# Performance work log

Measured on AMD Instinct MI355X. Metric: run time of the kernel, lower is better.

The kernel has to match this reference:

```python
import jax, jax.numpy as jnp
import numpy as np

NEG_INF = -1e9
LRELU_SLOPE = 0.2

B, C, FIN, FOUT = 8, 2048, 128, 64


def setup_inputs() -> dict:
    key = jax.random.key(0)
    k1, k2, k3, k4 = jax.random.split(key, 4)
    H = jax.random.normal(k1, (B, C, FIN), dtype=jnp.float32)
    A = jax.random.randint(k2, (B, C, C), 0, 2, dtype=jnp.int32)
    W = jax.random.normal(k3, (FIN, FOUT), dtype=jnp.float32)
    a = jax.random.normal(k4, (2 * FOUT,), dtype=jnp.float32)
    return {"H": H, "A": A, "W": W, "a": a}


def reference(H, A, W, a):
    # Wh: [B, C, F]
    Wh = jnp.einsum("bcf,fo->bco", H, W)
    F = Wh.shape[-1]
    a1, a2 = a[:F], a[F:]
    # e_ij = a . concat(Wh_i, Wh_j) = (Wh_i . a1) + (Wh_j . a2)
    # -> never materialize the (B,C,C,2F) concat tensor; same math.
    s1 = jnp.einsum("bcf,f->bc", Wh, a1)  # [B, C] contribution of node i
    s2 = jnp.einsum("bcf,f->bc", Wh, a2)  # [B, C] contribution of node j
    e = jax.nn.leaky_relu(s1[:, :, None] + s2[:, None, :], LRELU_SLOPE)  # [B,C,C]
    mask = (A > 0) | jnp.eye(A.shape[-1], dtype=bool)[None]
    e = jnp.where(mask, e, NEG_INF)
    alpha = jax.nn.softmax(e, axis=-1)
    # dropout omitted (eval mode) for a deterministic correctness baseline
    out = jax.nn.relu(jnp.einsum("bij,bjf->bif", alpha, Wh))
    return out
```

## Files before the change

kernel.cpp:

```cpp
#include <hip/hip_runtime.h>

#define NB 8
#define NC 2048
#define KIN 128
#define NF 64

#define WTSTRIDE 136
#define RSTRIDE 68
#define MOFF 60.0f
#define LOG2E 1.44269504088896340736f

typedef float floatx4_t __attribute__((ext_vector_type(4)));
typedef __bf16 bf16x8_t __attribute__((ext_vector_type(8)));
typedef unsigned short ushort8_t __attribute__((ext_vector_type(8)));

static __device__ __forceinline__ unsigned short f2bf(float f) {
  union { float f; unsigned int u; } v; v.f = f;
  unsigned int u = v.u;
  u += 0x7FFFu + ((u >> 16) & 1u);
  return (unsigned short)(u >> 16);
}

static __device__ __forceinline__ float lrelu(float x) {
  return fmaxf(x, 0.2f * x);
}

__global__ __launch_bounds__(256, 4) void k1_prep(
    const float* __restrict__ H, const float* __restrict__ W,
    const float* __restrict__ avec,
    float* __restrict__ s1g, float* __restrict__ s2g,
    unsigned short* __restrict__ WhT)
{
  __shared__ unsigned short WTsh[NF * WTSTRIDE];
  __shared__ float w1sh[KIN];
  __shared__ float w2sh[KIN];

  const int t = threadIdx.x;
  const int b = blockIdx.x >> 7;
  const int c0 = (blockIdx.x & 127) * 16;

  for (int i = t; i < KIN * NF; i += 256) {
    int k = i >> 6, f = i & 63;
    WTsh[f * WTSTRIDE + k] = f2bf(W[i]);
  }
  if (t < KIN) {
    float acc1 = 0.f, acc2 = 0.f;
    const float* wr = W + t * NF;
#pragma unroll
    for (int f = 0; f < NF; ++f) {
      float wv = wr[f];
      acc1 += wv * avec[f];
      acc2 += wv * avec[NF + f];
    }
    w1sh[t] = acc1;
    w2sh[t] = acc2;
  }
  __syncthreads();

  {
    const int r = t >> 4;
    const int x = t & 15;
    const float* hp = H + (size_t)(b * NC + c0 + r) * KIN + x * 8;
    float4 h0 = *(const float4*)(hp);
    float4 h1 = *(const float4*)(hp + 4);
    float4 u10 = *(const float4*)(w1sh + x * 8);
    float4 u11 = *(const float4*)(w1sh + x * 8 + 4);
    float4 u20 = *(const float4*)(w2sh + x * 8);
    float4 u21 = *(const float4*)(w2sh + x * 8 + 4);
    float p1 = h0.x * u10.x + h0.y * u10.y + h0.z * u10.z + h0.w * u10.w
             + h1.x * u11.x + h1.y * u11.y + h1.z * u11.z + h1.w * u11.w;
    float p2 = h0.x * u20.x + h0.y * u20.y + h0.z * u20.z + h0.w * u20.w
             + h1.x * u21.x + h1.y * u21.y + h1.z * u21.z + h1.w * u21.w;
#pragma unroll
    for (int off = 1; off < 16; off <<= 1) {
      p1 += __shfl_xor(p1, off);
      p2 += __shfl_xor(p2, off);
    }
    if (x == 0) {
      s1g[b * NC + c0 + r] = p1;
      s2g[b * NC + c0 + r] = p2;
    }
  }

  const int wave = t >> 6;
  const int lane = t & 63;
  const int m = lane & 15;
  const int q = lane >> 4;
  floatx4_t acc = (floatx4_t){0.f, 0.f, 0.f, 0.f};

  const float* hb = H + (size_t)(b * NC + c0 + m) * KIN;
#pragma unroll
  for (int kt = 0; kt < 4; ++kt) {
    const int kbase = kt * 32 + q * 8;
    float4 h0 = *(const float4*)(hb + kbase);
    float4 h1 = *(const float4*)(hb + kbase + 4);
    ushort8_t bu;
    bu[0] = f2bf(h0.x); bu[1] = f2bf(h0.y); bu[2] = f2bf(h0.z); bu[3] = f2bf(h0.w);
    bu[4] = f2bf(h1.x); bu[5] = f2bf(h1.y); bu[6] = f2bf(h1.z); bu[7] = f2bf(h1.w);
    bf16x8_t bf = __builtin_bit_cast(bf16x8_t, bu);
    ushort8_t au = *(const ushort8_t*)(WTsh + (wave * 16 + m) * WTSTRIDE + kbase);
    bf16x8_t af = __builtin_bit_cast(bf16x8_t, au);
    acc = __builtin_amdgcn_mfma_f32_16x16x32_bf16(af, bf, acc, 0, 0, 0);
  }
#pragma unroll
  for (int i2 = 0; i2 < 4; ++i2) {
    const int f = wave * 16 + q * 4 + i2;
    WhT[(size_t)(b * NF + f) * NC + c0 + m] = f2bf(acc[i2]);
  }
}

__global__ __launch_bounds__(256, 4) void k2_attn(
    const int* __restrict__ A, const float* __restrict__ s1g,
    const float* __restrict__ s2g, const unsigned short* __restrict__ WhT,
    float* __restrict__ out)
{
  __shared__ float s2_sh[NC];
  __shared__ float s1_sh[16];
  __shared__ float wmax_sh[4];
  __shared__ float red_sh[4 * 16 * RSTRIDE];
  __shared__ float lsum_sh[4 * 16];

  const int t = threadIdx.x;
  const int b = blockIdx.x >> 7;
  const int i0 = (blockIdx.x & 127) * 16;
  const int wave = t >> 6;
  const int lane = t & 63;

  float lmax;
  {
    const float* sp = s2g + b * NC;
    float4 v0 = *(const float4*)(sp + t * 4);
    float4 v1 = *(const float4*)(sp + 1024 + t * 4);
    *(float4*)(s2_sh + t * 4) = v0;
    *(float4*)(s2_sh + 1024 + t * 4) = v1;
    lmax = fmaxf(fmaxf(fmaxf(v0.x, v0.y), fmaxf(v0.z, v0.w)),
                 fmaxf(fmaxf(v1.x, v1.y), fmaxf(v1.z, v1.w)));
#pragma unroll
    for (int off = 1; off < 64; off <<= 1)
      lmax = fmaxf(lmax, __shfl_xor(lmax, off));
    if (lane == 0) wmax_sh[wave] = lmax;
  }
  if (t < 16) s1_sh[t] = s1g[b * NC + i0 + t];
  __syncthreads();

  const float s2max =
      fmaxf(fmaxf(wmax_sh[0], wmax_sh[1]), fmaxf(wmax_sh[2], wmax_sh[3]));

  const int m = lane & 15;
  const int q = lane >> 4;
  const int gi = i0 + m;
  const float s1m = s1_sh[m];
  const float mmL = (lrelu(s1m + s2max) - MOFF) * LOG2E;
  const int* Ap = A + ((size_t)b * NC + gi) * NC;
  const unsigned short* whb = WhT + (size_t)b * NF * NC;

  ushort8_t ou;
  {
    const unsigned short ov = (m == 0) ? (unsigned short)0x3F80 : (unsigned short)0;
#pragma unroll
    for (int idx = 0; idx < 8; ++idx) ou[idx] = ov;
  }
  const bf16x8_t onesf = __builtin_bit_cast(bf16x8_t, ou);

  floatx4_t acc[4], accl;
#pragma unroll
  for (int nt = 0; nt < 4; ++nt) acc[nt] = (floatx4_t){0.f, 0.f, 0.f, 0.f};
  accl = (floatx4_t){0.f, 0.f, 0.f, 0.f};

  const int ktBeg = wave * 16;
  int4 abuf[2][2];
  {
    const int* ap0 = Ap + ktBeg * 32 + q * 8;
    abuf[0][0] = *(const int4*)ap0;
    abuf[0][1] = *(const int4*)(ap0 + 4);
    const int* ap1 = ap0 + 32;
    abuf[1][0] = *(const int4*)ap1;
    abuf[1][1] = *(const int4*)(ap1 + 4);
  }

#pragma unroll 2
  for (int kk = 0; kk < 16; ++kk) {
    const int kt = ktBeg + kk;
    const int jq = kt * 32 + q * 8;
    const int cur = kk & 1;
    const int4 a0 = abuf[cur][0];
    const int4 a1 = abuf[cur][1];
    if (kk + 2 < 16) {
      const int* ap = Ap + (kt + 2) * 32 + q * 8;
      abuf[cur][0] = *(const int4*)ap;
      abuf[cur][1] = *(const int4*)(ap + 4);
    }
    ushort8_t whc[4];
#pragma unroll
    for (int nt = 0; nt < 4; ++nt)
      whc[nt] = *(const ushort8_t*)(whb + (size_t)(nt * 16 + m) * NC + jq);

    float4 s0 = *(const float4*)(s2_sh + jq);
    float4 s1v = *(const float4*)(s2_sh + jq + 4);
    const float sv[8] = {s0.x, s0.y, s0.z, s0.w, s1v.x, s1v.y, s1v.z, s1v.w};
    const int av[8] = {a0.x, a0.y, a0.z, a0.w, a1.x, a1.y, a1.z, a1.w};
    const int d = gi - jq;
    unsigned int pu[8];
#pragma unroll
    for (int idx = 0; idx < 8; ++idx) {
      float x = s1m + sv[idx];
      float p = __builtin_amdgcn_exp2f(fmaf(lrelu(x), LOG2E, -mmL));
      bool keep = (av[idx] > 0) || (d == idx);
      p = keep ? p : 0.0f;
      pu[idx] = __builtin_bit_cast(unsigned int, p);
    }
    uint4 pk;
    pk.x = __builtin_amdgcn_perm(pu[1], pu[0], 0x07060302u);
    pk.y = __builtin_amdgcn_perm(pu[3], pu[2], 0x07060302u);
    pk.z = __builtin_amdgcn_perm(pu[5], pu[4], 0x07060302u);
    pk.w = __builtin_amdgcn_perm(pu[7], pu[6], 0x07060302u);
    const bf16x8_t af = __builtin_bit_cast(bf16x8_t, pk);
#pragma unroll
    for (int nt = 0; nt < 4; ++nt) {
      bf16x8_t bf = __builtin_bit_cast(bf16x8_t, whc[nt]);
      acc[nt] = __builtin_amdgcn_mfma_f32_16x16x32_bf16(af, bf, acc[nt], 0, 0, 0);
    }
    accl = __builtin_amdgcn_mfma_f32_16x16x32_bf16(af, onesf, accl, 0, 0, 0);
  }

#pragma unroll
  for (int nt = 0; nt < 4; ++nt) {
#pragma unroll
    for (int i2 = 0; i2 < 4; ++i2) {
      red_sh[wave * (16 * RSTRIDE) + (q * 4 + i2) * RSTRIDE + nt * 16 + m] =
          acc[nt][i2];
    }
  }
  if (m == 0) {
#pragma unroll
    for (int i2 = 0; i2 < 4; ++i2)
      lsum_sh[wave * 16 + q * 4 + i2] = accl[i2];
  }
  __syncthreads();

  {
    const int row = t >> 4;
    const int f0 = (t & 15) * 4;
    float4 v = {0.f, 0.f, 0.f, 0.f};
    float ls = 0.f;
#pragma unroll
    for (int w = 0; w < 4; ++w) {
      const float* rp = red_sh + w * (16 * RSTRIDE) + row * RSTRIDE + f0;
      float4 vv = *(const float4*)rp;
      v.x += vv.x; v.y += vv.y; v.z += vv.z; v.w += vv.w;
      ls += lsum_sh[w * 16 + row];
    }
    const float inv = 1.0f / ls;
    float4 o;
    o.x = fmaxf(v.x * inv, 0.f);
    o.y = fmaxf(v.y * inv, 0.f);
    o.z = fmaxf(v.z * inv, 0.f);
    o.w = fmaxf(v.w * inv, 0.f);
    *(float4*)(out + (size_t)(b * NC + i0 + row) * NF + f0) = o;
  }
}

extern "C" void kernel_launch(void* const* d_in, const int* in_sizes, int n_in,
                              void* d_out, int out_size, void* d_ws, size_t ws_size,
                              hipStream_t stream) {
  const float* H = (const float*)d_in[0];
  const int* A = (const int*)d_in[1];
  const float* W = (const float*)d_in[2];
  const float* avec = (const float*)d_in[3];
  float* out = (float*)d_out;

  char* ws = (char*)d_ws;
  unsigned short* WhT = (unsigned short*)ws;
  float* s1 = (float*)(ws + (size_t)NB * NF * NC * 2);
  float* s2 = s1 + NB * NC;

  k1_prep<<<dim3(NB * (NC / 16)), dim3(256), 0, stream>>>(H, W, avec, s1, s2, WhT);
  k2_attn<<<dim3(NB * (NC / 16)), dim3(256), 0, stream>>>(A, s1, s2, WhT, out);
}
```

Before: 232.2 us.

## Stage adjacency mask as packed bits in shared memory before attention loop

Each block now reads its 16 rows of the int32 adjacency matrix up front with coalesced full-row loads. It packs each row into a byte bitmask (diagonal included) in shared memory, and the main MFMA loop reads one mask byte per lane instead of two int4 global loads. This replaces scattered 32-byte-per-lane A loads interleaved with compute by a contiguous prologue, and drops the register double-buffering of A. The risk is that the A traffic is no longer overlapped with the exp/MFMA work, so the prologue latency becomes exposed. It also adds about 4 KB of LDS per block, which could lower occupancy.

Result: slower. 239.7 us (+3.2%).

```diff
diff --git a/kernel.cpp b/kernel.cpp
--- a/kernel.cpp
+++ b/kernel.cpp
@@ -7,6 +7,7 @@
 
 #define WTSTRIDE 136
 #define RSTRIDE 68
+#define MROW 264
 #define MOFF 60.0f
 #define LOG2E 1.44269504088896340736f
 
@@ -115,6 +116,7 @@
     float* __restrict__ out)
 {
   __shared__ float s2_sh[NC];
+  __shared__ unsigned char mask_sh[16 * MROW];
   __shared__ float s1_sh[16];
   __shared__ float wmax_sh[4];
   __shared__ float red_sh[4 * 16 * RSTRIDE];
@@ -141,6 +143,33 @@
     if (lane == 0) wmax_sh[wave] = lmax;
   }
   if (t < 16) s1_sh[t] = s1g[b * NC + i0 + t];
+
+#pragma unroll 2
+  for (int rr = 0; rr < 4; ++rr) {
+    const int row = wave * 4 + rr;
+    const int gRow = i0 + row;
+    const int* arow = A + ((size_t)b * NC + gRow) * NC;
+#pragma unroll
+    for (int span = 0; span < 4; ++span) {
+      const int cbase = span * 512 + lane * 8;
+      int4 a0 = *(const int4*)(arow + cbase);
+      int4 a1 = *(const int4*)(arow + cbase + 4);
+      unsigned int byte = 0;
+      byte |= (a0.x > 0 || cbase + 0 == gRow) ? 1u : 0u;
+      byte |= (a0.y > 0 || cbase + 1 == gRow) ? 2u : 0u;
+      byte |= (a0.z > 0 || cbase + 2 == gRow) ? 4u : 0u;
+      byte |= (a0.w > 0 || cbase + 3 == gRow) ? 8u : 0u;
+      byte |= (a1.x > 0 || cbase + 4 == gRow) ? 16u : 0u;
+      byte |= (a1.y > 0 || cbase + 5 == gRow) ? 32u : 0u;
+      byte |= (a1.z > 0 || cbase + 6 == gRow) ? 64u : 0u;
+      byte |= (a1.w > 0 || cbase + 7 == gRow) ? 128u : 0u;
+      unsigned int v = byte;
+      v |= ((unsigned int)__shfl_xor((int)v, 1)) << 8;
+      v |= ((unsigned int)__shfl_xor((int)v, 2)) << 16;
+      if ((lane & 3) == 0)
+        *(unsigned int*)(mask_sh + row * MROW + span * 64 + lane) = v;
+    }
+  }
   __syncthreads();
 
   const float s2max =
@@ -148,10 +177,8 @@
 
   const int m = lane & 15;
   const int q = lane >> 4;
-  const int gi = i0 + m;
   const float s1m = s1_sh[m];
   const float mmL = (lrelu(s1m + s2max) - MOFF) * LOG2E;
-  const int* Ap = A + ((size_t)b * NC + gi) * NC;
   const unsigned short* whb = WhT + (size_t)b * NF * NC;
 
   ushort8_t ou;
@@ -168,28 +195,10 @@
   accl = (floatx4_t){0.f, 0.f, 0.f, 0.f};
 
   const int ktBeg = wave * 16;
-  int4 abuf[2][2];
-  {
-    const int* ap0 = Ap + ktBeg * 32 + q * 8;
-    abuf[0][0] = *(const int4*)ap0;
-    abuf[0][1] = *(const int4*)(ap0 + 4);
-    const int* ap1 = ap0 + 32;
-    abuf[1][0] = *(const int4*)ap1;
-    abuf[1][1] = *(const int4*)(ap1 + 4);
-  }
-
-#pragma unroll 2
   for (int kk = 0; kk < 16; ++kk) {
     const int kt = ktBeg + kk;
     const int jq = kt * 32 + q * 8;
-    const int cur = kk & 1;
-    const int4 a0 = abuf[cur][0];
-    const int4 a1 = abuf[cur][1];
-    if (kk + 2 < 16) {
-      const int* ap = Ap + (kt + 2) * 32 + q * 8;
-      abuf[cur][0] = *(const int4*)ap;
-      abuf[cur][1] = *(const int4*)(ap + 4);
-    }
+    const unsigned int mb = mask_sh[m * MROW + kt * 4 + q];
     ushort8_t whc[4];
 #pragma unroll
     for (int nt = 0; nt < 4; ++nt)
@@ -198,22 +207,19 @@
     float4 s0 = *(const float4*)(s2_sh + jq);
     float4 s1v = *(const float4*)(s2_sh + jq + 4);
     const float sv[8] = {s0.x, s0.y, s0.z, s0.w, s1v.x, s1v.y, s1v.z, s1v.w};
-    const int av[8] = {a0.x, a0.y, a0.z, a0.w, a1.x, a1.y, a1.z, a1.w};
-    const int d = gi - jq;
-    unsigned int pu[8];
-#pragma unroll
-    for (int idx = 0; idx < 8; ++idx) {
-      float x = s1m + sv[idx];
-      float p = __builtin_amdgcn_exp2f(fmaf(lrelu(x), LOG2E, -mmL));
-      bool keep = (av[idx] > 0) || (d == idx);
-      p = keep ? p : 0.0f;
-      pu[idx] = __builtin_bit_cast(unsigned int, p);
-    }
     uint4 pk;
-    pk.x = __builtin_amdgcn_perm(pu[1], pu[0], 0x07060302u);
-    pk.y = __builtin_amdgcn_perm(pu[3], pu[2], 0x07060302u);
-    pk.z = __builtin_amdgcn_perm(pu[5], pu[4], 0x07060302u);
-    pk.w = __builtin_amdgcn_perm(pu[7], pu[6], 0x07060302u);
+#pragma unroll
+    for (int pair = 0; pair < 4; ++pair) {
+      float p0 = __builtin_amdgcn_exp2f(
+          fmaf(lrelu(s1m + sv[2 * pair]), LOG2E, -mmL));
+      float p1 = __builtin_amdgcn_exp2f(
+          fmaf(lrelu(s1m + sv[2 * pair + 1]), LOG2E, -mmL));
+      p0 = (mb & (1u << (2 * pair))) ? p0 : 0.0f;
+      p1 = (mb & (2u << (2 * pair))) ? p1 : 0.0f;
+      pk[pair] = __builtin_amdgcn_perm(__builtin_bit_cast(unsigned int, p1),
+                                       __builtin_bit_cast(unsigned int, p0),
+                                       0x07060302u);
+    }
     const bf16x8_t af = __builtin_bit_cast(bf16x8_t, pk);
 #pragma unroll
     for (int nt = 0; nt < 4; ++nt) {
```
